# Performance work log

Measured on AMD Instinct MI355X. Metric: run time of the kernel, lower is better.

## Reference

```python
import jax, jax.numpy as jnp
import numpy as np

CLIP_VAL = 32

def setup_inputs() -> dict:
    key = jax.random.key(0)
    ks = jax.random.split(key, 8)
    B, T, D_MODEL, H, DK = 4, 1024, 1024, 16, 64
    s = 0.02  # small init scale, glorot-like magnitude
    return {
        "query": jax.random.normal(ks[0], (B, T, D_MODEL), jnp.float32),
        "value": jax.random.normal(ks[1], (B, T, D_MODEL), jnp.float32),
        "W_Q": jax.random.normal(ks[2], (H, D_MODEL, DK), jnp.float32) * s,
        "W_K": jax.random.normal(ks[3], (H, D_MODEL, DK), jnp.float32) * s,
        "W_V": jax.random.normal(ks[4], (H, D_MODEL, DK), jnp.float32) * s,
        "W_O": jax.random.normal(ks[5], (H, DK, D_MODEL), jnp.float32) * s,
        "emb_Q": jax.random.normal(ks[6], (2 * CLIP_VAL + 1, DK), jnp.float32) * s,
        "emb_S": jax.random.normal(ks[7], (2 * CLIP_VAL + 1, DK), jnp.float32) * s,
    }

def reference(query, value, W_Q, W_K, W_V, W_O, emb_Q, emb_S):
    # query/value: (B, T, D_Model); per-head weights: (H, D_Model, Dk)
    T = query.shape[1]
    Dk = W_Q.shape[-1]
    sqrt_D = jnp.sqrt(jnp.asarray(Dk, query.dtype))

    # relative position index matrix: (T, T) ints in [0, 2*clip]
    tau = jnp.arange(T)
    rel = (jnp.clip(tau[None, :] - tau[:, None], -CLIP_VAL, CLIP_VAL) + CLIP_VAL)
    eQ = emb_Q[rel]  # (T, T, Dk) relative key embedding
    eS = emb_S[rel]  # (T, T, Dv) relative value embedding

    qW = jnp.einsum('btm,hmd->bhtd', query, W_Q)  # (B,H,T,Dk)
    kW = jnp.einsum('btm,hmd->bhtd', value, W_K)
    vW = jnp.einsum('btm,hmd->bhtd', value, W_V)

    # content scores + relative-query bias, both scaled by 1/sqrt(Dk)
    scores = (jnp.einsum('bhtd,bhsd->bhts', qW, kW)
              + jnp.einsum('bhtd,tsd->bhts', qW, eQ)) / sqrt_D
    p = jax.nn.softmax(scores, axis=-1)  # (B,H,T,T)

    # value combination + relative-value term
    heads = (jnp.einsum('bhts,bhsd->bhtd', p, vW)
             + jnp.einsum('bhts,tsd->bhtd', p, eS))

    # per-head output projection then sum over heads
    out = jnp.einsum('bhtd,hdm->btm', heads, W_O)  # (B,T,D_Model)
    return out
```

## Files before the change

### kernel.cpp

```cpp
#include <hip/hip_runtime.h>
#include <math.h>


typedef _Float16 f16;
typedef f16 half8 __attribute__((ext_vector_type(8)));
typedef f16 half4v __attribute__((ext_vector_type(4)));
typedef float f32x4 __attribute__((ext_vector_type(4)));

__global__ __launch_bounds__(256) void prep(
    const float* __restrict__ q, const float* __restrict__ v,
    const float* __restrict__ W0, const float* __restrict__ W1,
    const float* __restrict__ W2, const float* __restrict__ WO,
    f16* __restrict__ q16, f16* __restrict__ Wt16, f16* __restrict__ WOt16) {
    __shared__ float tile[64][65];
    const int bx = blockIdx.x;
    const int t = threadIdx.x;
    if (bx < 8192) {
        int i = (bx * 256 + t) * 4;
        const float* s = (i < 4194304) ? (q + i) : (v + (i - 4194304));
        float4 x = *(const float4*)s;
        half4v h = {(f16)x.x, (f16)x.y, (f16)x.z, (f16)x.w};
        *(half4v*)&q16[i] = h;
        return;
    }
    const int c = t & 63, r4 = t >> 6;
    const int n = t >> 2, kc = (t & 3) * 16;
    if (bx < 8960) {
        const int idx = bx - 8192;
        const int z = idx >> 4, k0 = (idx & 15) * 64;
        const float* src = ((z < 16) ? W0 : (z < 32) ? W1 : W2) + (size_t)(z & 15) * 65536;
        f16* out = Wt16 + (size_t)z * 65536;
#pragma unroll
        for (int p = 0; p < 16; ++p)
            tile[r4 + p * 4][c] = src[(size_t)(k0 + r4 + p * 4) * 64 + c];
        __syncthreads();
        f16 buf[16];
#pragma unroll
        for (int i = 0; i < 16; ++i) buf[i] = (f16)tile[kc + i][n];
        *(half8*)&out[(size_t)n * 1024 + k0 + kc] = *(half8*)&buf[0];
        *(half8*)&out[(size_t)n * 1024 + k0 + kc + 8] = *(half8*)&buf[8];
        return;
    }
    {
        const int idx = bx - 8960;
        const int k0 = (idx & 15) * 64, n0 = (idx >> 4) * 64;
#pragma unroll
        for (int p = 0; p < 16; ++p)
            tile[r4 + p * 4][c] = WO[(size_t)(k0 + r4 + p * 4) * 1024 + n0 + c];
        __syncthreads();
        f16 buf[16];
#pragma unroll
        for (int i = 0; i < 16; ++i) buf[i] = (f16)tile[kc + i][n];
        *(half8*)&WOt16[(size_t)(n0 + n) * 1024 + k0 + kc] = *(half8*)&buf[0];
        *(half8*)&WOt16[(size_t)(n0 + n) * 1024 + k0 + kc + 8] = *(half8*)&buf[8];
    }
}

template <int MODE>
__global__ __launch_bounds__(256) void mfma_gemm(
    const f16* __restrict__ Aq, const f16* __restrict__ Av,
    const f16* __restrict__ Bt, float* __restrict__ C,
    f16* __restrict__ oQ, f16* __restrict__ oK, f16* __restrict__ oVt) {
    constexpr int K = 1024;
    const int n0 = blockIdx.x * 128;
    const int m0 = blockIdx.y * 128;
    const f16* Abase = (MODE == 0) ? ((n0 < 1024) ? Aq : Av) : Aq;

    __shared__ f16 lds[16384];

    const int tid = threadIdx.x;
    const int l = tid & 63, wv = tid >> 6;
    const int rseg = l >> 3;
    const int g = (l & 7) ^ rseg;
    const int rowBase = (wv & 1) * 64;
    const f16* gSrc = (wv < 2) ? (Abase + (size_t)m0 * K) : (Bt + (size_t)n0 * K);
    const f16* gLane = gSrc + (size_t)(rowBase + rseg) * K + g * 8;
    const int ldsRow0 = ((wv < 2) ? 0 : 128) + rowBase;

    const int fr = l & 15, fq = l >> 4, sw = fr & 7;
    const int mi2 = wv & 1, ni2 = wv >> 1;
    int aOff[4], bOff[4];
#pragma unroll
    for (int i = 0; i < 4; ++i) {
        bOff[i] = (mi2 * 64 + i * 16 + fr) * 128;
        aOff[i] = (128 + ni2 * 64 + i * 16 + fr) * 128;
    }

    f32x4 acc[4][4];
#pragma unroll
    for (int i = 0; i < 4; ++i)
#pragma unroll
        for (int j = 0; j < 4; ++j) acc[i][j] = {0.f, 0.f, 0.f, 0.f};

    for (int k0 = 0; k0 < K; k0 += 64) {
#pragma unroll
        for (int i = 0; i < 8; ++i) {
            const f16* src = gLane + (size_t)i * 8 * K + k0;
            __builtin_amdgcn_global_load_lds(
                (const __attribute__((address_space(1))) unsigned int*)src,
                (__attribute__((address_space(3))) unsigned int*)&lds[(ldsRow0 + i * 8) * 64],
                16, 0, 0);
        }
        __syncthreads();
#pragma unroll
        for (int kk = 0; kk < 2; ++kk) {
            const int glq = kk * 4 + fq;
            const int sgl = (glq ^ sw) * 16;
            half8 aF[4], bF[4];
#pragma unroll
            for (int i = 0; i < 4; ++i) {
                aF[i] = *(const half8*)((const char*)lds + aOff[i] + sgl);
                bF[i] = *(const half8*)((const char*)lds + bOff[i] + sgl);
            }
#pragma unroll
            for (int mi = 0; mi < 4; ++mi)
#pragma unroll
                for (int ni = 0; ni < 4; ++ni)
                    acc[mi][ni] = __builtin_amdgcn_mfma_f32_16x16x32_f16(
                        aF[ni], bF[mi], acc[mi][ni], 0, 0, 0);
        }
        __syncthreads();
    }
#pragma unroll
    for (int mi = 0; mi < 4; ++mi) {
        const int m = m0 + mi2 * 64 + mi * 16 + fr;
#pragma unroll
        for (int ni = 0; ni < 4; ++ni) {
            const int n = n0 + ni2 * 64 + ni * 16 + 4 * fq;
            if (MODE == 1) {
                *(f32x4*)(C + (size_t)m * 1024 + n) = acc[mi][ni];
            } else {
                const int w = n >> 10, h = (n >> 6) & 15, d = n & 63;
                const int b = m >> 10, t = m & 1023;
                const size_t bh = (size_t)(b * 16 + h);
                f32x4 a = acc[mi][ni];
                if (w == 0) {
                    half4v hv = {(f16)(a[0] * 0.125f), (f16)(a[1] * 0.125f),
                                 (f16)(a[2] * 0.125f), (f16)(a[3] * 0.125f)};
                    *(half4v*)&oQ[bh * 65536 + (size_t)t * 64 + d] = hv;
                } else if (w == 1) {
                    half4v hv = {(f16)a[0], (f16)a[1], (f16)a[2], (f16)a[3]};
                    *(half4v*)&oK[bh * 65536 + (size_t)t * 64 + d] = hv;
                } else {
#pragma unroll
                    for (int r = 0; r < 4; ++r)
                        oVt[bh * 65536 + (size_t)(d + r) * 1024 + t] = (f16)a[r];
                }
            }
        }
    }
}

__global__ __launch_bounds__(256, 3) void attn_kernel(
    const f16* __restrict__ q16a, const f16* __restrict__ k16,
    const f16* __restrict__ vt16, const float* __restrict__ embQ,
    const float* __restrict__ embS, f16* __restrict__ heads16) {
    const int bh = blockIdx.x;
    const int t0 = blockIdx.y * 64;
    const f16* qg = q16a + (size_t)bh * 65536;
    const f16* kg = k16  + (size_t)bh * 65536;
    const f16* vg = vt16 + (size_t)bh * 65536;

    __shared__ f16 Kt[64][72];
    __shared__ f16 Vt[64][72];
    __shared__ f16 Pt[64][72];
    __shared__ f16 band[64][66];
    __shared__ f16 qEl[80][72];

    const int tid = threadIdx.x;
    const int wv = tid >> 6, lane = tid & 63;
    const int tloc = lane & 15, quad = lane >> 4;
    const int trow = wv * 16 + tloc;
    const int tg = t0 + trow;

    for (int idx = tid; idx < 640; idx += 256) {
        const int row = idx >> 3, seg = idx & 7;
        half8 h;
        if (row < 65) {
            const float* s = embQ + row * 64 + seg * 8;
#pragma unroll
            for (int j = 0; j < 8; ++j) h[j] = (f16)s[j];
        } else {
#pragma unroll
            for (int j = 0; j < 8; ++j) h[j] = (f16)0.f;
        }
        *(half8*)&qEl[row][seg * 8] = h;
    }
    for (int i = tid; i < 64 * 66; i += 256) (&band[0][0])[i] = (f16)(-1.0e4f);

    half8 qf[2];
    qf[0] = *(const half8*)&qg[(size_t)tg * 64 + quad * 8];
    qf[1] = *(const half8*)&qg[(size_t)tg * 64 + 32 + quad * 8];
    __syncthreads();

    {
        f32x4 qacc[5];
#pragma unroll
        for (int rt = 0; rt < 5; ++rt) qacc[rt] = {0.f, 0.f, 0.f, 0.f};
#pragma unroll
        for (int kk = 0; kk < 2; ++kk)
#pragma unroll
            for (int rt = 0; rt < 5; ++rt) {
                half8 ef = *(const half8*)&qEl[rt * 16 + tloc][kk * 32 + quad * 8];
                qacc[rt] = __builtin_amdgcn_mfma_f32_16x16x32_f16(
                    ef, qf[kk], qacc[rt], 0, 0, 0);
            }
        __syncthreads();
#pragma unroll
        for (int rt = 0; rt < 5; ++rt)
#pragma unroll
            for (int j = 0; j < 4; ++j) {
                const int r = rt * 16 + quad * 4 + j;
                if (r < 65) qEl[r][trow] = (f16)qacc[rt][j];
            }
    }
    __syncthreads();
    const float qE0  = (float)qEl[0][trow];
    const float qE64 = (float)qEl[64][trow];

    float rs = 0.f, rsL = 0.f;
    f32x4 oacc[4];
#pragma unroll
    for (int nt = 0; nt < 4; ++nt) oacc[nt] = {0.f, 0.f, 0.f, 0.f};

    const int srow = tid >> 2, scol = (tid & 3) * 16;

    for (int j0 = 0; j0 < 1024; j0 += 64) {
        __syncthreads();
        {
            const f16* ks = kg + (size_t)(j0 + srow) * 64 + scol;
            const f16* vs = vg + (size_t)srow * 1024 + j0 + scol;
            half8 a0 = *(const half8*)ks, a1 = *(const half8*)(ks + 8);
            half8 b0 = *(const half8*)vs, b1 = *(const half8*)(vs + 8);
            *(half8*)&Kt[srow][scol] = a0; *(half8*)&Kt[srow][scol + 8] = a1;
            *(half8*)&Vt[srow][scol] = b0; *(half8*)&Vt[srow][scol + 8] = b1;
        }
        __syncthreads();
        f32x4 sacc[4];
#pragma unroll
        for (int mt = 0; mt < 4; ++mt) sacc[mt] = {0.f, 0.f, 0.f, 0.f};
#pragma unroll
        for (int kk = 0; kk < 2; ++kk)
#pragma unroll
            for (int mt = 0; mt < 4; ++mt) {
                half8 kf = *(const half8*)&Kt[mt * 16 + tloc][kk * 32 + quad * 8];
                sacc[mt] = __builtin_amdgcn_mfma_f32_16x16x32_f16(
                    kf, qf[kk], sacc[mt], 0, 0, 0);
            }
        const bool leftU  = (j0 <= t0 - 128);
        const bool rightU = (j0 >= t0 + 128);
        if (leftU | rightU) {
            const float bias = leftU ? qE0 : qE64;
            float ts = 0.f;
#pragma unroll
            for (int mt = 0; mt < 4; ++mt)
#pragma unroll
                for (int r = 0; r < 4; ++r) {
                    float p = __expf(sacc[mt][r] + bias);
                    sacc[mt][r] = p; ts += p;
                }
            rs += ts;
            if (leftU) rsL += ts;
        } else {
#pragma unroll
            for (int mt = 0; mt < 4; ++mt)
#pragma unroll
                for (int r = 0; r < 4; ++r) {
                    int ds = j0 + mt * 16 + quad * 4 + r - tg;
                    int dc = ds < -32 ? -32 : (ds > 32 ? 32 : ds);
                    float v = sacc[mt][r] + (float)qEl[dc + 32][trow];
                    float p = __expf(v);
                    sacc[mt][r] = p; rs += p;
                    if (ds <= -32) rsL += p;
                    if (ds >= -31 && ds <= 31) band[trow][ds + 31] = (f16)v;
                }
        }
#pragma unroll
        for (int mt = 0; mt < 4; ++mt) {
            half4v h = {(f16)sacc[mt][0], (f16)sacc[mt][1],
                        (f16)sacc[mt][2], (f16)sacc[mt][3]};
            *(half4v*)&Pt[trow][mt * 16 + quad * 4] = h;
        }
#pragma unroll
        for (int kk = 0; kk < 2; ++kk) {
            half8 pf = *(const half8*)&Pt[trow][kk * 32 + quad * 8];
#pragma unroll
            for (int nt = 0; nt < 4; ++nt) {
                half8 vf = *(const half8*)&Vt[nt * 16 + tloc][kk * 32 + quad * 8];
                oacc[nt] = __builtin_amdgcn_mfma_f32_16x16x32_f16(
                    pf, vf, oacc[nt], 0, 0, 0);
            }
        }
    }
    rs  += __shfl_xor(rs, 16);  rs  += __shfl_xor(rs, 32);
    rsL += __shfl_xor(rsL, 16); rsL += __shfl_xor(rsL, 32);

    float sumBand = 0.f;
    {
        f16 pb[16];
#pragma unroll
        for (int i = 0; i < 16; ++i) {
            int k = quad * 16 + i;
            float v;
            if (k == 63) v = rsL;
            else { v = __expf((float)band[trow][k]); sumBand += v; }
            pb[i] = (f16)v;
        }
        *(half8*)&Pt[trow][quad * 16] = *(half8*)&pb[0];
        *(half8*)&Pt[trow][quad * 16 + 8] = *(half8*)&pb[8];
    }
    sumBand += __shfl_xor(sumBand, 16);
    sumBand += __shfl_xor(sumBand, 32);
    const float sumR = rs - rsL - sumBand;

    __syncthreads();
    {
        const int d = tid & 63;
        const int kb = (tid >> 6) * 16;
#pragma unroll
        for (int i = 0; i < 16; ++i) {
            int k = kb + i;
            Kt[d][k] = (f16)embS[((k == 63) ? 0 : (k + 1)) * 64 + d];
        }
    }
    __syncthreads();
#pragma unroll
    for (int kk = 0; kk < 2; ++kk) {
        half8 pf = *(const half8*)&Pt[trow][kk * 32 + quad * 8];
#pragma unroll
        for (int nt = 0; nt < 4; ++nt) {
            half8 ef = *(const half8*)&Kt[nt * 16 + tloc][kk * 32 + quad * 8];
            oacc[nt] = __builtin_amdgcn_mfma_f32_16x16x32_f16(
                pf, ef, oacc[nt], 0, 0, 0);
        }
    }
    float lr4[4], sR4[4];
#pragma unroll
    for (int r = 0; r < 4; ++r) {
        lr4[r] = __shfl(rs,   (quad << 2) + r);
        sR4[r] = __shfl(sumR, (quad << 2) + r);
    }
    const int b = bh >> 4, h = bh & 15;
#pragma unroll
    for (int nt = 0; nt < 4; ++nt) {
        const int d = nt * 16 + tloc;
        const float e64 = embS[64 * 64 + d];
#pragma unroll
        for (int r = 0; r < 4; ++r) {
            const int tw = t0 + wv * 16 + (quad << 2) + r;
            float val = (oacc[nt][r] + sR4[r] * e64) / lr4[r];
            heads16[(size_t)(b * 1024 + tw) * 1024 + h * 64 + d] = (f16)val;
        }
    }
}

extern "C" void kernel_launch(void* const* d_in, const int* in_sizes, int n_in,
                              void* d_out, int out_size, void* d_ws, size_t ws_size,
                              hipStream_t stream) {
    const float* query = (const float*)d_in[0];
    const float* value = (const float*)d_in[1];
    const float* WQ   = (const float*)d_in[2];
    const float* WK   = (const float*)d_in[3];
    const float* WV   = (const float*)d_in[4];
    const float* WO   = (const float*)d_in[5];
    const float* embQ = (const float*)d_in[6];
    const float* embS = (const float*)d_in[7];
    float* out = (float*)d_out;

    f16* w0    = (f16*)d_ws;
    f16* q16   = w0;
    f16* v16   = w0 + 4194304;
    f16* Wt16  = w0 + 8388608;
    f16* WOt16 = w0 + 11534336;
    f16* q16a  = w0 + 12582912;
    f16* k16   = w0 + 16777216;
    f16* vt16  = w0 + 20971520;
    f16* h16   = w0 + 25165824;

    prep<<<9216, 256, 0, stream>>>(query, value, WQ, WK, WV, WO,
                                   q16, Wt16, WOt16);
    mfma_gemm<0><<<dim3(24, 32), 256, 0, stream>>>(q16, v16, Wt16, nullptr,
                                                   q16a, k16, vt16);
    attn_kernel<<<dim3(64, 16), 256, 0, stream>>>(q16a, k16, vt16, embQ, embS, h16);
    mfma_gemm<1><<<dim3(8, 32), 256, 0, stream>>>(h16, h16, WOt16, out,
                                                  nullptr, nullptr, nullptr);
}
```

Before: 213.0 us.

## Rewrite attention kernel with 128-row tiles, 32x32 MFMA and direct-to-LDS loads

The attention kernel now handles 128 query rows per block instead of 64, so each K/V tile loaded from global memory is reused across twice as many queries. It switches to 32x32x16 MFMA, keeps P in registers via cross-lane shuffles instead of staging it through LDS, and uses global_load_lds with XOR-swizzled layouts to avoid bank conflicts. Output is staged through LDS so the global stores are coalesced. The trade-off is more registers and LDS per block (launch bounds drop to 2 blocks), half as many blocks, and no double-buffering of K/V loads.

```diff
diff --git a/kernel.cpp b/kernel.cpp
--- a/kernel.cpp
+++ b/kernel.cpp
@@ -6,6 +6,7 @@
 typedef f16 half8 __attribute__((ext_vector_type(8)));
 typedef f16 half4v __attribute__((ext_vector_type(4)));
 typedef float f32x4 __attribute__((ext_vector_type(4)));
+typedef float f32x16 __attribute__((ext_vector_type(16)));
 
 __global__ __launch_bounds__(256) void prep(
     const float* __restrict__ q, const float* __restrict__ v,
@@ -151,207 +152,237 @@
     }
 }
 
-__global__ __launch_bounds__(256, 3) void attn_kernel(
+__global__ __launch_bounds__(256, 2) void attn_kernel(
     const f16* __restrict__ q16a, const f16* __restrict__ k16,
     const f16* __restrict__ vt16, const float* __restrict__ embQ,
     const float* __restrict__ embS, f16* __restrict__ heads16) {
     const int bh = blockIdx.x;
-    const int t0 = blockIdx.y * 64;
+    const int t0 = blockIdx.y * 128;
     const f16* qg = q16a + (size_t)bh * 65536;
-    const f16* kg = k16  + (size_t)bh * 65536;
+    const f16* kg = k16 + (size_t)bh * 65536;
     const f16* vg = vt16 + (size_t)bh * 65536;
 
-    __shared__ f16 Kt[64][72];
-    __shared__ f16 Vt[64][72];
-    __shared__ f16 Pt[64][72];
-    __shared__ f16 band[64][66];
-    __shared__ f16 qEl[80][72];
+    __shared__ f16 Kt[4096];
+    __shared__ f16 Vt[4096];
+    __shared__ f16 qEl[66 * 136];
+    __shared__ f16 band[128 * 72];
+    __shared__ float e64s[64];
 
     const int tid = threadIdx.x;
     const int wv = tid >> 6, lane = tid & 63;
-    const int tloc = lane & 15, quad = lane >> 4;
-    const int trow = wv * 16 + tloc;
-    const int tg = t0 + trow;
-
-    for (int idx = tid; idx < 640; idx += 256) {
-        const int row = idx >> 3, seg = idx & 7;
-        half8 h;
+    const int tl32 = lane & 31, h = lane >> 5;
+    const int tl = wv * 32 + tl32;
+    const int tg = t0 + tl;
+
+    f16* embQs = band;
+    for (int idx = tid; idx < 768; idx += 256) {
+        const int row = idx >> 3, p = idx & 7, g = p ^ (row & 7);
+        half8 hv;
         if (row < 65) {
-            const float* s = embQ + row * 64 + seg * 8;
-#pragma unroll
-            for (int j = 0; j < 8; ++j) h[j] = (f16)s[j];
+            const float* s = embQ + row * 64 + g * 8;
+#pragma unroll
+            for (int j = 0; j < 8; ++j) hv[j] = (f16)s[j];
         } else {
 #pragma unroll
-            for (int j = 0; j < 8; ++j) h[j] = (f16)0.f;
-        }
-        *(half8*)&qEl[row][seg * 8] = h;
-    }
-    for (int i = tid; i < 64 * 66; i += 256) (&band[0][0])[i] = (f16)(-1.0e4f);
-
-    half8 qf[2];
-    qf[0] = *(const half8*)&qg[(size_t)tg * 64 + quad * 8];
-    qf[1] = *(const half8*)&qg[(size_t)tg * 64 + 32 + quad * 8];
+            for (int j = 0; j < 8; ++j) hv[j] = (f16)0.f;
+        }
+        *(half8*)&embQs[row * 64 + p * 8] = hv;
+    }
+    half8 qf[4];
+#pragma unroll
+    for (int ks = 0; ks < 4; ++ks)
+        qf[ks] = *(const half8*)&qg[(size_t)tg * 64 + (2 * ks + h) * 8];
     __syncthreads();
-
     {
-        f32x4 qacc[5];
-#pragma unroll
-        for (int rt = 0; rt < 5; ++rt) qacc[rt] = {0.f, 0.f, 0.f, 0.f};
-#pragma unroll
-        for (int kk = 0; kk < 2; ++kk)
-#pragma unroll
-            for (int rt = 0; rt < 5; ++rt) {
-                half8 ef = *(const half8*)&qEl[rt * 16 + tloc][kk * 32 + quad * 8];
-                qacc[rt] = __builtin_amdgcn_mfma_f32_16x16x32_f16(
-                    ef, qf[kk], qacc[rt], 0, 0, 0);
-            }
-        __syncthreads();
-#pragma unroll
-        for (int rt = 0; rt < 5; ++rt)
-#pragma unroll
-            for (int j = 0; j < 4; ++j) {
-                const int r = rt * 16 + quad * 4 + j;
-                if (r < 65) qEl[r][trow] = (f16)qacc[rt][j];
-            }
-    }
+        f32x16 qacc[3];
+#pragma unroll
+        for (int mt = 0; mt < 3; ++mt)
+#pragma unroll
+            for (int r = 0; r < 16; ++r) qacc[mt][r] = 0.f;
+#pragma unroll
+        for (int ks = 0; ks < 4; ++ks)
+#pragma unroll
+            for (int mt = 0; mt < 3; ++mt) {
+                const int row = tl32 + 32 * mt;
+                const int p = (2 * ks + h) ^ (row & 7);
+                half8 ef = *(const half8*)&embQs[row * 64 + p * 8];
+                qacc[mt] = __builtin_amdgcn_mfma_f32_32x32x16_f16(
+                    ef, qf[ks], qacc[mt], 0, 0, 0);
+            }
+        __syncthreads();
+#pragma unroll
+        for (int mt = 0; mt < 3; ++mt)
+#pragma unroll
+            for (int r = 0; r < 16; ++r) {
+                const int rr = (r & 3) + 8 * (r >> 2) + 4 * h + 32 * mt;
+                if (rr < 65) qEl[rr * 136 + tl] = (f16)qacc[mt][r];
+            }
+    }
+    for (int idx = tid; idx < 1152; idx += 256) {
+        half8 hv;
+#pragma unroll
+        for (int j = 0; j < 8; ++j) hv[j] = (f16)(-1.0e4f);
+        *(half8*)&band[idx * 8] = hv;
+    }
+    if (tid < 64) e64s[tid] = embS[64 * 64 + tid];
     __syncthreads();
-    const float qE0  = (float)qEl[0][trow];
-    const float qE64 = (float)qEl[64][trow];
+    const float qE0 = (float)qEl[tl];
+    const float qE64 = (float)qEl[64 * 136 + tl];
 
     float rs = 0.f, rsL = 0.f;
-    f32x4 oacc[4];
-#pragma unroll
-    for (int nt = 0; nt < 4; ++nt) oacc[nt] = {0.f, 0.f, 0.f, 0.f};
-
-    const int srow = tid >> 2, scol = (tid & 3) * 16;
+    f32x16 oacc[2];
+#pragma unroll
+    for (int dt = 0; dt < 2; ++dt)
+#pragma unroll
+        for (int r = 0; r < 16; ++r) oacc[dt][r] = 0.f;
 
     for (int j0 = 0; j0 < 1024; j0 += 64) {
-        __syncthreads();
-        {
-            const f16* ks = kg + (size_t)(j0 + srow) * 64 + scol;
-            const f16* vs = vg + (size_t)srow * 1024 + j0 + scol;
-            half8 a0 = *(const half8*)ks, a1 = *(const half8*)(ks + 8);
-            half8 b0 = *(const half8*)vs, b1 = *(const half8*)(vs + 8);
-            *(half8*)&Kt[srow][scol] = a0; *(half8*)&Kt[srow][scol + 8] = a1;
-            *(half8*)&Vt[srow][scol] = b0; *(half8*)&Vt[srow][scol + 8] = b1;
-        }
-        __syncthreads();
-        f32x4 sacc[4];
-#pragma unroll
-        for (int mt = 0; mt < 4; ++mt) sacc[mt] = {0.f, 0.f, 0.f, 0.f};
-#pragma unroll
-        for (int kk = 0; kk < 2; ++kk)
-#pragma unroll
-            for (int mt = 0; mt < 4; ++mt) {
-                half8 kf = *(const half8*)&Kt[mt * 16 + tloc][kk * 32 + quad * 8];
-                sacc[mt] = __builtin_amdgcn_mfma_f32_16x16x32_f16(
-                    kf, qf[kk], sacc[mt], 0, 0, 0);
-            }
-        const bool leftU  = (j0 <= t0 - 128);
-        const bool rightU = (j0 >= t0 + 128);
-        if (leftU | rightU) {
-            const float bias = leftU ? qE0 : qE64;
+#pragma unroll
+        for (int i = 0; i < 2; ++i) {
+            const int rt = wv * 16 + i * 8 + (lane >> 3);
+            const int g = (lane & 7) ^ (rt & 7);
+            __builtin_amdgcn_global_load_lds(
+                (const __attribute__((address_space(1))) unsigned int*)
+                    (kg + (size_t)(j0 + rt) * 64 + g * 8),
+                (__attribute__((address_space(3))) unsigned int*)
+                    &Kt[(wv * 16 + i * 8) * 64], 16, 0, 0);
+            __builtin_amdgcn_global_load_lds(
+                (const __attribute__((address_space(1))) unsigned int*)
+                    (vg + (size_t)rt * 1024 + j0 + g * 8),
+                (__attribute__((address_space(3))) unsigned int*)
+                    &Vt[(wv * 16 + i * 8) * 64], 16, 0, 0);
+        }
+        __syncthreads();
+        f32x16 sacc[2];
+#pragma unroll
+        for (int mt = 0; mt < 2; ++mt)
+#pragma unroll
+            for (int r = 0; r < 16; ++r) sacc[mt][r] = 0.f;
+#pragma unroll
+        for (int ks = 0; ks < 4; ++ks)
+#pragma unroll
+            for (int mt = 0; mt < 2; ++mt) {
+                const int row = tl32 + 32 * mt;
+                const int p = (2 * ks + h) ^ (row & 7);
+                half8 kf = *(const half8*)&Kt[row * 64 + p * 8];
+                sacc[mt] = __builtin_amdgcn_mfma_f32_32x32x16_f16(
+                    kf, qf[ks], sacc[mt], 0, 0, 0);
+            }
+        const int dj = j0 - t0;
+        if (dj <= -128 || dj >= 192) {
+            const float bias = (dj < 0) ? qE0 : qE64;
             float ts = 0.f;
 #pragma unroll
-            for (int mt = 0; mt < 4; ++mt)
-#pragma unroll
-                for (int r = 0; r < 4; ++r) {
-                    float p = __expf(sacc[mt][r] + bias);
-                    sacc[mt][r] = p; ts += p;
+            for (int mt = 0; mt < 2; ++mt)
+#pragma unroll
+                for (int r = 0; r < 16; ++r) {
+                    float pe = __expf(sacc[mt][r] + bias);
+                    sacc[mt][r] = pe; ts += pe;
                 }
             rs += ts;
-            if (leftU) rsL += ts;
+            if (dj < 0) rsL += ts;
         } else {
 #pragma unroll
-            for (int mt = 0; mt < 4; ++mt)
-#pragma unroll
-                for (int r = 0; r < 4; ++r) {
-                    int ds = j0 + mt * 16 + quad * 4 + r - tg;
-                    int dc = ds < -32 ? -32 : (ds > 32 ? 32 : ds);
-                    float v = sacc[mt][r] + (float)qEl[dc + 32][trow];
-                    float p = __expf(v);
-                    sacc[mt][r] = p; rs += p;
-                    if (ds <= -32) rsL += p;
-                    if (ds >= -31 && ds <= 31) band[trow][ds + 31] = (f16)v;
+            for (int mt = 0; mt < 2; ++mt)
+#pragma unroll
+                for (int r = 0; r < 16; ++r) {
+                    const int sg = j0 + 32 * mt + (r & 3) + 8 * (r >> 2) + 4 * h;
+                    const int ds = sg - tg;
+                    const int dc = ds < -32 ? -32 : (ds > 32 ? 32 : ds);
+                    float v = sacc[mt][r] + (float)qEl[(dc + 32) * 136 + tl];
+                    if (ds >= -31 && ds <= 31) band[tl * 72 + ds + 31] = (f16)v;
+                    float pe = __expf(v);
+                    sacc[mt][r] = pe; rs += pe;
+                    if (ds <= -32) rsL += pe;
                 }
         }
 #pragma unroll
-        for (int mt = 0; mt < 4; ++mt) {
-            half4v h = {(f16)sacc[mt][0], (f16)sacc[mt][1],
-                        (f16)sacc[mt][2], (f16)sacc[mt][3]};
-            *(half4v*)&Pt[trow][mt * 16 + quad * 4] = h;
-        }
-#pragma unroll
-        for (int kk = 0; kk < 2; ++kk) {
-            half8 pf = *(const half8*)&Pt[trow][kk * 32 + quad * 8];
-#pragma unroll
-            for (int nt = 0; nt < 4; ++nt) {
-                half8 vf = *(const half8*)&Vt[nt * 16 + tloc][kk * 32 + quad * 8];
-                oacc[nt] = __builtin_amdgcn_mfma_f32_16x16x32_f16(
-                    pf, vf, oacc[nt], 0, 0, 0);
-            }
-        }
-    }
-    rs  += __shfl_xor(rs, 16);  rs  += __shfl_xor(rs, 32);
-    rsL += __shfl_xor(rsL, 16); rsL += __shfl_xor(rsL, 32);
-
+        for (int ks = 0; ks < 4; ++ks) {
+            const int mtile = ks >> 1, rb = (ks & 1) * 8;
+            float ex[4];
+#pragma unroll
+            for (int c = 0; c < 4; ++c) {
+                float send = (h == 0) ? sacc[mtile][rb + 4 + c]
+                                      : sacc[mtile][rb + c];
+                ex[c] = __shfl_xor(send, 32);
+            }
+            half8 pf;
+#pragma unroll
+            for (int j = 0; j < 4; ++j)
+                pf[j] = (f16)((h == 0) ? sacc[mtile][rb + j] : ex[j]);
+#pragma unroll
+            for (int j = 0; j < 4; ++j)
+                pf[4 + j] = (f16)((h == 0) ? ex[j] : sacc[mtile][rb + 4 + j]);
+#pragma unroll
+            for (int dt = 0; dt < 2; ++dt) {
+                const int row = tl32 + 32 * dt;
+                const int p = (2 * ks + h) ^ (row & 7);
+                half8 vf = *(const half8*)&Vt[row * 64 + p * 8];
+                oacc[dt] = __builtin_amdgcn_mfma_f32_32x32x16_f16(
+                    vf, pf, oacc[dt], 0, 0, 0);
+            }
+        }
+        __syncthreads();
+    }
+    rs += __shfl_xor(rs, 32);
+    rsL += __shfl_xor(rsL, 32);
     float sumBand = 0.f;
-    {
-        f16 pb[16];
-#pragma unroll
-        for (int i = 0; i < 16; ++i) {
-            int k = quad * 16 + i;
+#pragma unroll
+    for (int c = 0; c < 4; ++c) {
+        const int kb = 32 * h + 8 * c;
+        half8 bv = *(const half8*)&band[tl * 72 + kb];
+        half8 ev;
+#pragma unroll
+        for (int j = 0; j < 8; ++j) {
+            const int k = kb + j;
             float v;
             if (k == 63) v = rsL;
-            else { v = __expf((float)band[trow][k]); sumBand += v; }
-            pb[i] = (f16)v;
-        }
-        *(half8*)&Pt[trow][quad * 16] = *(half8*)&pb[0];
-        *(half8*)&Pt[trow][quad * 16 + 8] = *(half8*)&pb[8];
-    }
-    sumBand += __shfl_xor(sumBand, 16);
+            else { v = __expf((float)bv[j]); sumBand += v; }
+            ev[j] = (f16)v;
+        }
+        *(half8*)&band[tl * 72 + kb] = ev;
+    }
     sumBand += __shfl_xor(sumBand, 32);
     const float sumR = rs - rsL - sumBand;
-
+    for (int idx = tid; idx < 512; idx += 256) {
+        const int d = idx >> 3, p = idx & 7, g = p ^ (d & 7);
+        half8 hv;
+#pragma unroll
+        for (int j = 0; j < 8; ++j) {
+            const int k = g * 8 + j;
+            hv[j] = (f16)embS[((k == 63) ? 0 : (k + 1)) * 64 + d];
+        }
+        *(half8*)&Kt[d * 64 + p * 8] = hv;
+    }
     __syncthreads();
-    {
-        const int d = tid & 63;
-        const int kb = (tid >> 6) * 16;
-#pragma unroll
-        for (int i = 0; i < 16; ++i) {
-            int k = kb + i;
-            Kt[d][k] = (f16)embS[((k == 63) ? 0 : (k + 1)) * 64 + d];
+#pragma unroll
+    for (int ks = 0; ks < 4; ++ks) {
+        half8 pf = *(const half8*)&band[tl * 72 + 16 * ks + 8 * h];
+#pragma unroll
+        for (int dt = 0; dt < 2; ++dt) {
+            const int row = tl32 + 32 * dt;
+            const int p = (2 * ks + h) ^ (row & 7);
+            half8 ef = *(const half8*)&Kt[row * 64 + p * 8];
+            oacc[dt] = __builtin_amdgcn_mfma_f32_32x32x16_f16(
+                ef, pf, oacc[dt], 0, 0, 0);
         }
     }
     __syncthreads();
-#pragma unroll
-    for (int kk = 0; kk < 2; ++kk) {
-        half8 pf = *(const half8*)&Pt[trow][kk * 32 + quad * 8];
-#pragma unroll
-        for (int nt = 0; nt < 4; ++nt) {
-            half8 ef = *(const half8*)&Kt[nt * 16 + tloc][kk * 32 + quad * 8];
-            oacc[nt] = __builtin_amdgcn_mfma_f32_16x16x32_f16(
-                pf, ef, oacc[nt], 0, 0, 0);
-        }
-    }
-    float lr4[4], sR4[4];
-#pragma unroll
-    for (int r = 0; r < 4; ++r) {
-        lr4[r] = __shfl(rs,   (quad << 2) + r);
-        sR4[r] = __shfl(sumR, (quad << 2) + r);
-    }
-    const int b = bh >> 4, h = bh & 15;
-#pragma unroll
-    for (int nt = 0; nt < 4; ++nt) {
-        const int d = nt * 16 + tloc;
-        const float e64 = embS[64 * 64 + d];
-#pragma unroll
-        for (int r = 0; r < 4; ++r) {
-            const int tw = t0 + wv * 16 + (quad << 2) + r;
-            float val = (oacc[nt][r] + sR4[r] * e64) / lr4[r];
-            heads16[(size_t)(b * 1024 + tw) * 1024 + h * 64 + d] = (f16)val;
-        }
-    }
+    const float inv = 1.0f / rs;
+#pragma unroll
+    for (int dt = 0; dt < 2; ++dt)
+#pragma unroll
+        for (int r = 0; r < 16; ++r) {
+            const int d = (r & 3) + 8 * (r >> 2) + 4 * h + 32 * dt;
+            band[tl * 72 + d] = (f16)((oacc[dt][r] + sumR * e64s[d]) * inv);
+        }
+    __syncthreads();
+    const int b = bh >> 4, hh = bh & 15;
+    const int row = tid >> 1, cb = (tid & 1) * 32;
+    f16* dst = heads16 + ((size_t)(b * 1024 + t0 + row) * 1024) + hh * 64 + cb;
+#pragma unroll
+    for (int c = 0; c < 4; ++c)
+        *(half8*)&dst[c * 8] = *(const half8*)&band[row * 72 + cb + c * 8];
 }
 
 extern "C" void kernel_launch(void* const* d_in, const int* in_sizes, int n_in,
@@ -381,7 +412,7 @@
                                    q16, Wt16, WOt16);
     mfma_gemm<0><<<dim3(24, 32), 256, 0, stream>>>(q16, v16, Wt16, nullptr,
                                                    q16a, k16, vt16);
-    attn_kernel<<<dim3(64, 16), 256, 0, stream>>>(q16a, k16, vt16, embQ, embS, h16);
+    attn_kernel<<<dim3(64, 8), 256, 0, stream>>>(q16a, k16, vt16, embQ, embS, h16);
     mfma_gemm<1><<<dim3(8, 32), 256, 0, stream>>>(h16, h16, WOt16, out,
                                                   nullptr, nullptr, nullptr);
 }
```

Result: no change. 212.1 us (-0.4%).
